# Performance work log

Hardware: AMD Instinct MI355X
Metric: run time of the kernel (lower is better)

## Reference

```python
import jax, jax.numpy as jnp
import numpy as np

# ---- production-scale dims (see shape_source) ----
B, S = 256, 512            # batch, seq_len
HD, INTD = 512, 256        # hidden_dim, hidden_dim // dim_div
N_TEST, N_ITEM, N_TAG = 1500, 9454, 912
N_USER = 7442
GE_ROWS = N_USER + N_ITEM  # LightGCN table: users + items
N_CONT = 3


def _layer_norm(x, g, b, eps=1e-5):
    mu = jnp.mean(x, axis=-1, keepdims=True)
    var = jnp.var(x, axis=-1, keepdims=True)
    return (x - mu) * jax.lax.rsqrt(var + eps) * g + b


def setup_inputs() -> dict:
    key = jax.random.key(0)
    ks = jax.random.split(key, 14)
    f = lambda k, shp, s=0.02: jax.random.normal(k, shp, dtype=jnp.float32) * s
    return {
        # forward data args
        "cate_testId": jax.random.randint(ks[0], (B, S), 0, N_TEST),
        "cate_itemId": jax.random.randint(ks[1], (B, S), 0, N_ITEM),
        "cate_tag": jax.random.randint(ks[2], (B, S), 0, N_TAG),
        "cont_feats": jax.random.normal(ks[3], (B, S, N_CONT), dtype=jnp.float32),
        "interaction": jax.random.randint(ks[4], (B, S), 0, 3),
        # learned parameters
        "emb_interaction": f(ks[5], (3, INTD)),
        "emb_testId": f(ks[6], (N_TEST + 1, INTD)),
        "emb_itemId": f(ks[7], (N_ITEM + 1, INTD)),
        "emb_tag": f(ks[8], (N_TAG + 1, INTD)),
        "graph_table": f(ks[9], (GE_ROWS, HD)),           # pre-trained LightGCN embedding (np.load in torch)
        "graph_W": f(ks[10], (HD, INTD), 0.05),            # graph_linear (in, out) layout
        "graph_b": jnp.zeros((INTD,), jnp.float32),
        "comb_W": f(ks[11], (INTD * 5, HD // 2)),          # intd*(3 cate + 1 graph + interaction)
        "comb_b": jnp.zeros((HD // 2,), jnp.float32),
        "comb_g": jnp.ones((HD // 2,), jnp.float32),
        "comb_beta": jnp.zeros((HD // 2,), jnp.float32),
        "cont_W": f(ks[12], (N_CONT, HD // 2), 0.1),
        "cont_b": jnp.zeros((HD // 2,), jnp.float32),
        "cont_g": jnp.ones((HD // 2,), jnp.float32),
        "cont_beta": jnp.zeros((HD // 2,), jnp.float32),
    }


def reference(cate_testId, cate_itemId, cate_tag, cont_feats, interaction,
              emb_interaction, emb_testId, emb_itemId, emb_tag,
              graph_table, graph_W, graph_b,
              comb_W, comb_b, comb_g, comb_beta,
              cont_W, cont_b, cont_g, cont_beta):
    # categorical + interaction embedding lookups: [B,S,INTD] each
    e_int = emb_interaction[interaction]
    e_test = emb_testId[cate_testId]
    e_item = emb_itemId[cate_itemId]
    e_tag = emb_tag[cate_tag]
    # graph embedding path: fused gather (replaces the CPU python-loop gather)
    # indexes row (n_userID - 1 + value) of the LightGCN table, value from data[0]=testId
    g = graph_table[N_USER - 1 + cate_testId]          # [B,S,HD]
    g = g @ graph_W + graph_b                          # [B,S,INTD]
    embed = jnp.concatenate([e_int, e_test, e_item, e_tag, g], axis=-1)  # [B,S,5*INTD]
    cate = _layer_norm(embed @ comb_W + comb_b, comb_g, comb_beta)       # [B,S,HD//2]
    cont = _layer_norm(cont_feats @ cont_W + cont_b, cont_g, cont_beta)  # [B,S,HD//2]
    return jnp.concatenate([cate, cont], axis=-1)                        # [B,S,HD]
```

## Files before the change

kernel.cpp:

```cpp
#include <hip/hip_runtime.h>
#include <hip/hip_bf16.h>

#define NTOK   (256 * 512)
#define N_USER 7442

using bf16 = __hip_bfloat16;
typedef float f32x4 __attribute__((ext_vector_type(4)));

static __device__ __forceinline__ float4 ld4(const float* p) {
    return *reinterpret_cast<const float4*>(p);
}
static __device__ __forceinline__ float bfl(unsigned u) {
    union { unsigned u; float f; } c; c.u = u << 16; return c.f;
}
static __device__ __forceinline__ float bfh(unsigned u) {
    union { unsigned u; float f; } c; c.u = u & 0xFFFF0000u; return c.f;
}
static __device__ __forceinline__ void st_nt4(float* p, float x, float y, float z, float w) {
    f32x4 v; v.x = x; v.y = y; v.z = z; v.w = w;
    __builtin_nontemporal_store(v, reinterpret_cast<f32x4*>(p));
}
static __device__ __forceinline__ float rnd_bf(float x) {
    return __bfloat162float(__float2bfloat16(x));
}
static __device__ __forceinline__ void st_bf4(bf16* dst, float4 v) {
    union { bf16 h[4]; uint2 u; } pk;
    pk.h[0] = __float2bfloat16(v.x);
    pk.h[1] = __float2bfloat16(v.y);
    pk.h[2] = __float2bfloat16(v.z);
    pk.h[3] = __float2bfloat16(v.w);
    *reinterpret_cast<uint2*>(dst) = pk.u;
}

template <int CTRL, int ROW_MASK>
static __device__ __forceinline__ float dpp_add(float x) {
    const int sh = __builtin_amdgcn_update_dpp(0, __float_as_int(x), CTRL, ROW_MASK, 0xf, true);
    return x + __int_as_float(sh);
}
static __device__ __forceinline__ float wave_sum(float x) {
    x = dpp_add<0x111, 0xf>(x);
    x = dpp_add<0x112, 0xf>(x);
    x = dpp_add<0x114, 0xf>(x);
    x = dpp_add<0x118, 0xf>(x);
    x = dpp_add<0x142, 0xa>(x);
    x = dpp_add<0x143, 0xc>(x);
    return __int_as_float(__builtin_amdgcn_readlane(__float_as_int(x), 63));
}
static __device__ __forceinline__ float dot4(float4 a, float4 b) {
    return a.x * b.x + a.y * b.y + a.z * b.z + a.w * b.w;
}

#define NB_TESTG 188
#define NB_ITEM  591
#define NB_TAG   58
#define NB_INT   1
#define NB_PC    (NB_TESTG + NB_ITEM + NB_TAG + NB_INT)
#define NB_CONT  4096
#define NB_A     (NB_PC + NB_CONT)

__global__ __launch_bounds__(128) void precompute_cont_kernel(
    const float* __restrict__ emb_int,  const float* __restrict__ emb_test,
    const float* __restrict__ emb_item, const float* __restrict__ emb_tag,
    const float* __restrict__ graph_tab, const float* __restrict__ graph_W,
    const float* __restrict__ graph_b,
    const float* __restrict__ comb_W,   const float* __restrict__ comb_b,
    const float* __restrict__ cont_feats,
    const float* __restrict__ cont_W,   const float* __restrict__ cont_b,
    const float* __restrict__ cont_g,   const float* __restrict__ cont_beta,
    bf16* __restrict__ Pint, bf16* __restrict__ Ptestg,
    bf16* __restrict__ Pitem, bf16* __restrict__ Ptag,
    float* __restrict__ Rint, float* __restrict__ Rtestg,
    float* __restrict__ Ritem, float* __restrict__ Rtag,
    float* __restrict__ out) {
    __shared__ float lds[6400];
    const int tid  = threadIdx.x;
    const int w    = tid >> 6;
    const int lane = tid & 63;
    const int c    = lane * 4;
    const int b    = blockIdx.x;

    if (b >= NB_PC) {
        const float4 w0  = ld4(cont_W + 0 * 256 + c);
        const float4 w1  = ld4(cont_W + 1 * 256 + c);
        const float4 w2  = ld4(cont_W + 2 * 256 + c);
        const float4 cb  = ld4(cont_b + c);
        const float4 g42 = ld4(cont_g + c);
        const float4 b42 = ld4(cont_beta + c);

        const float inv256 = 1.f / 256.f;
        const float M0  = wave_sum(w0.x + w0.y + w0.z + w0.w) * inv256;
        const float M1  = wave_sum(w1.x + w1.y + w1.z + w1.w) * inv256;
        const float M2  = wave_sum(w2.x + w2.y + w2.z + w2.w) * inv256;
        const float M3  = wave_sum(cb.x + cb.y + cb.z + cb.w) * inv256;
        const float P00 = wave_sum(dot4(w0, w0)) * inv256;
        const float P11 = wave_sum(dot4(w1, w1)) * inv256;
        const float P22 = wave_sum(dot4(w2, w2)) * inv256;
        const float P33 = wave_sum(dot4(cb, cb)) * inv256;
        const float P01 = wave_sum(dot4(w0, w1)) * inv256;
        const float P02 = wave_sum(dot4(w0, w2)) * inv256;
        const float P12 = wave_sum(dot4(w1, w2)) * inv256;
        const float P03 = wave_sum(dot4(w0, cb)) * inv256;
        const float P13 = wave_sum(dot4(w1, cb)) * inv256;
        const float P23 = wave_sum(dot4(w2, cb)) * inv256;

        const int wid = (b - NB_PC) * 2 + w;
        const int t0  = wid * 16;
        for (int k4 = 0; k4 < 4; ++k4) {
            const int tb = t0 + k4 * 4;
            const float4 cf0 = ld4(cont_feats + (size_t)tb * 3);
            const float4 cf1 = ld4(cont_feats + (size_t)tb * 3 + 4);
            const float4 cf2 = ld4(cont_feats + (size_t)tb * 3 + 8);
            const float cf[12] = {cf0.x, cf0.y, cf0.z, cf0.w,
                                  cf1.x, cf1.y, cf1.z, cf1.w,
                                  cf2.x, cf2.y, cf2.z, cf2.w};
            #pragma unroll
            for (int j = 0; j < 4; ++j) {
                const int t = tb + j;
                const float c0 = cf[j * 3 + 0];
                const float c1 = cf[j * 3 + 1];
                const float c2 = cf[j * 3 + 2];
                const float mu2 = c0 * M0 + c1 * M1 + c2 * M2 + M3;
                const float e2  = c0 * c0 * P00 + c1 * c1 * P11 + c2 * c2 * P22 + P33
                                + 2.f * (c0 * c1 * P01 + c0 * c2 * P02 + c1 * c2 * P12
                                       + c0 * P03 + c1 * P13 + c2 * P23);
                const float inv2 = rsqrtf(e2 - mu2 * mu2 + 1e-5f);

                const float ux = c0 * w0.x + c1 * w1.x + c2 * w2.x + cb.x;
                const float uy = c0 * w0.y + c1 * w1.y + c2 * w2.y + cb.y;
                const float uz = c0 * w0.z + c1 * w1.z + c2 * w2.z + cb.z;
                const float uw = c0 * w0.w + c1 * w1.w + c2 * w2.w + cb.w;

                st_nt4(out + (size_t)t * 512 + 256 + c,
                       (ux - mu2) * inv2 * g42.x + b42.x,
                       (uy - mu2) * inv2 * g42.y + b42.y,
                       (uz - mu2) * inv2 * g42.z + b42.z,
                       (uw - mu2) * inv2 * g42.w + b42.w);
            }
        }
        return;
    }

    const float* W0 = comb_W;
    const float* W1 = comb_W + 256 * 256;
    const float* W2 = comb_W + 512 * 256;
    const float* W3 = comb_W + 768 * 256;
    const float* W4 = comb_W + 1024 * 256;

    if (b < NB_TESTG) {
        const int row0 = b * 8;
        const int nr   = min(8, 1500 - row0);

        for (int i = tid; i < 1024; i += 128) {
            const int r = i >> 7, m4 = (i & 127) * 4;
            const int rr = min(r, nr - 1);
            *reinterpret_cast<float4*>(&lds[r * 512 + m4]) =
                ld4(graph_tab + (size_t)(N_USER - 1 + row0 + rr) * 512 + m4);
        }
        __syncthreads();

        float4 acc[8];
        #pragma unroll
        for (int r = 0; r < 8; ++r) acc[r] = float4{0.f, 0.f, 0.f, 0.f};
        for (int m = w * 256; m < w * 256 + 256; m += 4) {
            const float4 wv0 = ld4(graph_W + (m + 0) * 256 + c);
            const float4 wv1 = ld4(graph_W + (m + 1) * 256 + c);
            const float4 wv2 = ld4(graph_W + (m + 2) * 256 + c);
            const float4 wv3 = ld4(graph_W + (m + 3) * 256 + c);
            #pragma unroll
            for (int r = 0; r < 8; ++r) {
                const float4 e = ld4(&lds[r * 512 + m]);
                acc[r].x += e.x * wv0.x + e.y * wv1.x + e.z * wv2.x + e.w * wv3.x;
                acc[r].y += e.x * wv0.y + e.y * wv1.y + e.z * wv2.y + e.w * wv3.y;
                acc[r].z += e.x * wv0.z + e.y * wv1.z + e.z * wv2.z + e.w * wv3.z;
                acc[r].w += e.x * wv0.w + e.y * wv1.w + e.z * wv2.w + e.w * wv3.w;
            }
        }
        __syncthreads();

        if (w == 0) {
            #pragma unroll
            for (int r = 0; r < 8; ++r)
                *reinterpret_cast<float4*>(&lds[4096 + r * 256 + c]) = acc[r];
        }
        __syncthreads();
        if (w == 1) {
            #pragma unroll
            for (int r = 0; r < 8; ++r) {
                float4 t = ld4(&lds[4096 + r * 256 + c]);
                t.x += acc[r].x; t.y += acc[r].y; t.z += acc[r].z; t.w += acc[r].w;
                *reinterpret_cast<float4*>(&lds[4096 + r * 256 + c]) = t;
            }
        }
        for (int i = tid; i < 512; i += 128) {
            const int r = i >> 6, m4 = (i & 63) * 4;
            const int rr = min(r, nr - 1);
            *reinterpret_cast<float4*>(&lds[r * 256 + m4]) =
                ld4(emb_test + (size_t)(row0 + rr) * 256 + m4);
        }
        __syncthreads();

        float4 acc2[8];
        float4 bacc = float4{0.f, 0.f, 0.f, 0.f};
        #pragma unroll
        for (int r = 0; r < 8; ++r) acc2[r] = float4{0.f, 0.f, 0.f, 0.f};
        for (int m = w * 128; m < w * 128 + 128; m += 4) {
            const float4 w40 = ld4(W4 + (m + 0) * 256 + c);
            const float4 w41 = ld4(W4 + (m + 1) * 256 + c);
            const float4 w42 = ld4(W4 + (m + 2) * 256 + c);
            const float4 w43 = ld4(W4 + (m + 3) * 256 + c);
            const float4 w10 = ld4(W1 + (m + 0) * 256 + c);
            const float4 w11 = ld4(W1 + (m + 1) * 256 + c);
            const float4 w12 = ld4(W1 + (m + 2) * 256 + c);
            const float4 w13 = ld4(W1 + (m + 3) * 256 + c);
            const float gb0 = graph_b[m + 0], gb1 = graph_b[m + 1];
            const float gb2 = graph_b[m + 2], gb3 = graph_b[m + 3];
            bacc.x += gb0 * w40.x + gb1 * w41.x + gb2 * w42.x + gb3 * w43.x;
            bacc.y += gb0 * w40.y + gb1 * w41.y + gb2 * w42.y + gb3 * w43.y;
            bacc.z += gb0 * w40.z + gb1 * w41.z + gb2 * w42.z + gb3 * w43.z;
            bacc.w += gb0 * w40.w + gb1 * w41.w + gb2 * w42.w + gb3 * w43.w;
            #pragma unroll
            for (int r = 0; r < 8; ++r) {
                const float4 tv = ld4(&lds[4096 + r * 256 + m]);
                const float4 ev = ld4(&lds[r * 256 + m]);
                acc2[r].x += tv.x * w40.x + tv.y * w41.x + tv.z * w42.x + tv.w * w43.x
                           + ev.x * w10.x + ev.y * w11.x + ev.z * w12.x + ev.w * w13.x;
                acc2[r].y += tv.x * w40.y + tv.y * w41.y + tv.z * w42.y + tv.w * w43.y
                           + ev.x * w10.y + ev.y * w11.y + ev.z * w12.y + ev.w * w13.y;
                acc2[r].z += tv.x * w40.z + tv.y * w41.z + tv.z * w42.z + tv.w * w43.z
                           + ev.x * w10.z + ev.y * w11.z + ev.z * w12.z + ev.w * w13.z;
                acc2[r].w += tv.x * w40.w + tv.y * w41.w + tv.z * w42.w + tv.w * w43.w
                           + ev.x * w10.w + ev.y * w11.w + ev.z * w12.w + ev.w * w13.w;
            }
        }
        if (w == 0) {
            #pragma unroll
            for (int r = 0; r < 8; ++r)
                *reinterpret_cast<float4*>(&lds[2048 + r * 256 + c]) = acc2[r];
            *reinterpret_cast<float4*>(&lds[6144 + c]) = bacc;
        }
        __syncthreads();
        if (w == 1) {
            #pragma unroll
            for (int r = 0; r < 8; ++r) {
                float4 t = ld4(&lds[2048 + r * 256 + c]);
                t.x += acc2[r].x; t.y += acc2[r].y; t.z += acc2[r].z; t.w += acc2[r].w;
                *reinterpret_cast<float4*>(&lds[2048 + r * 256 + c]) = t;
            }
            float4 t = ld4(&lds[6144 + c]);
            t.x += bacc.x; t.y += bacc.y; t.z += bacc.z; t.w += bacc.w;
            *reinterpret_cast<float4*>(&lds[6144 + c]) = t;
        }
        __syncthreads();

        const float4 cbv = ld4(comb_b + c);
        const float4 bb  = ld4(&lds[6144 + c]);
        #pragma unroll
        for (int r4 = 0; r4 < 4; ++r4) {
            const int r = w * 4 + r4;
            float4 o = ld4(&lds[2048 + r * 256 + c]);
            o.x += bb.x + cbv.x;
            o.y += bb.y + cbv.y;
            o.z += bb.z + cbv.z;
            o.w += bb.w + cbv.w;
            const float rs = wave_sum(rnd_bf(o.x) + rnd_bf(o.y) + rnd_bf(o.z) + rnd_bf(o.w));
            if (r < nr) {
                st_bf4(Ptestg + (size_t)(row0 + r) * 256 + c, o);
                if (lane == 0) Rtestg[row0 + r] = rs;
            }
        }
    } else {
        const float* E; const float* W; bf16* P; float* R; int row0, Rn;
        const int sb = b - NB_TESTG;
        if (sb < NB_ITEM)               { E = emb_item; W = W2; P = Pitem; R = Ritem; row0 = sb * 16;             Rn = 9455; }
        else if (sb < NB_ITEM + NB_TAG) { E = emb_tag;  W = W3; P = Ptag;  R = Rtag;  row0 = (sb - NB_ITEM) * 16; Rn = 913;  }
        else                            { E = emb_int;  W = W0; P = Pint;  R = Rint;  row0 = 0;                   Rn = 3;    }
        const int nr = min(16, Rn - row0);

        for (int i = tid; i < 1024; i += 128) {
            const int r = i >> 6, m4 = (i & 63) * 4;
            const int rr = min(r, nr - 1);
            *reinterpret_cast<float4*>(&lds[r * 256 + m4]) =
                ld4(E + (size_t)(row0 + rr) * 256 + m4);
        }
        __syncthreads();

        float4 acc[16];
        #pragma unroll
        for (int r = 0; r < 16; ++r) acc[r] = float4{0.f, 0.f, 0.f, 0.f};
        for (int m = w * 128; m < w * 128 + 128; m += 4) {
            const float4 wv0 = ld4(W + (m + 0) * 256 + c);
            const float4 wv1 = ld4(W + (m + 1) * 256 + c);
            const float4 wv2 = ld4(W + (m + 2) * 256 + c);
            const float4 wv3 = ld4(W + (m + 3) * 256 + c);
            #pragma unroll
            for (int r = 0; r < 16; ++r) {
                const float4 e = ld4(&lds[r * 256 + m]);
                acc[r].x += e.x * wv0.x + e.y * wv1.x + e.z * wv2.x + e.w * wv3.x;
                acc[r].y += e.x * wv0.y + e.y * wv1.y + e.z * wv2.y + e.w * wv3.y;
                acc[r].z += e.x * wv0.z + e.y * wv1.z + e.z * wv2.z + e.w * wv3.z;
                acc[r].w += e.x * wv0.w + e.y * wv1.w + e.z * wv2.w + e.w * wv3.w;
            }
        }
        __syncthreads();

        if (w == 0) {
            #pragma unroll
            for (int r = 0; r < 16; ++r)
                *reinterpret_cast<float4*>(&lds[r * 256 + c]) = acc[r];
        }
        __syncthreads();
        if (w == 1) {
            #pragma unroll
            for (int r = 0; r < 16; ++r) {
                float4 t = ld4(&lds[r * 256 + c]);
                t.x += acc[r].x; t.y += acc[r].y; t.z += acc[r].z; t.w += acc[r].w;
                *reinterpret_cast<float4*>(&lds[r * 256 + c]) = t;
            }
        }
        __syncthreads();

        #pragma unroll
        for (int r8 = 0; r8 < 8; ++r8) {
            const int r = w * 8 + r8;
            const float4 o = ld4(&lds[r * 256 + c]);
            const float rs = wave_sum(rnd_bf(o.x) + rnd_bf(o.y) + rnd_bf(o.z) + rnd_bf(o.w));
            if (r < nr) {
                st_bf4(P + (size_t)(row0 + r) * 256 + c, o);
                if (lane == 0) R[row0 + r] = rs;
            }
        }
    }
}

__global__ __launch_bounds__(256) void main_cate_kernel(
    const int* __restrict__ testId, const int* __restrict__ itemId,
    const int* __restrict__ tagId,  const int* __restrict__ inter,
    const bf16* __restrict__ Pint, const bf16* __restrict__ Ptestg,
    const bf16* __restrict__ Pitem, const bf16* __restrict__ Ptag,
    const float* __restrict__ Rint, const float* __restrict__ Rtestg,
    const float* __restrict__ Ritem, const float* __restrict__ Rtag,
    const float* __restrict__ comb_g, const float* __restrict__ comb_beta,
    float* __restrict__ out) {
    const int wid  = blockIdx.x * 4 + (threadIdx.x >> 6);
    const int lane = threadIdx.x & 63;
    const int c    = lane * 4;

    const float4 g4 = ld4(comb_g + c);
    const float4 b4 = ld4(comb_beta + c);
    const uint2 p0 = *reinterpret_cast<const uint2*>(Pint + 0 * 256 + c);
    const uint2 p1 = *reinterpret_cast<const uint2*>(Pint + 1 * 256 + c);
    const uint2 p2 = *reinterpret_cast<const uint2*>(Pint + 2 * 256 + c);
    const float ri0 = Rint[0], ri1 = Rint[1], ri2 = Rint[2];

    const int tb = wid * 4;
    const int4 tiv = *reinterpret_cast<const int4*>(testId + tb);
    const int4 iiv = *reinterpret_cast<const int4*>(itemId + tb);
    const int4 tgv = *reinterpret_cast<const int4*>(tagId  + tb);
    const int4 ivv = *reinterpret_cast<const int4*>(inter  + tb);
    const int tis[4] = {tiv.x, tiv.y, tiv.z, tiv.w};
    const int iis[4] = {iiv.x, iiv.y, iiv.z, iiv.w};
    const int tgs[4] = {tgv.x, tgv.y, tgv.z, tgv.w};
    const int ivs[4] = {ivv.x, ivv.y, ivv.z, ivv.w};

    uint2 gT[4], gI[4], gG[4];
    float sT[4], sI[4], sG[4];
    #pragma unroll
    for (int j = 0; j < 4; ++j) {
        gT[j] = *reinterpret_cast<const uint2*>(Ptestg + (size_t)tis[j] * 256 + c);
        gI[j] = *reinterpret_cast<const uint2*>(Pitem  + (size_t)iis[j] * 256 + c);
        gG[j] = *reinterpret_cast<const uint2*>(Ptag   + (size_t)tgs[j] * 256 + c);
        sT[j] = Rtestg[tis[j]];
        sI[j] = Ritem[iis[j]];
        sG[j] = Rtag[tgs[j]];
    }

    #pragma unroll
    for (int j = 0; j < 4; ++j) {
        const int t = tb + j;

        uint2 u0;
        u0.x = ivs[j] == 0 ? p0.x : (ivs[j] == 1 ? p1.x : p2.x);
        u0.y = ivs[j] == 0 ? p0.y : (ivs[j] == 1 ? p1.y : p2.y);
        const float sInt = ivs[j] == 0 ? ri0 : (ivs[j] == 1 ? ri1 : ri2);

        const float vx = bfl(u0.x) + bfl(gT[j].x) + bfl(gI[j].x) + bfl(gG[j].x);
        const float vy = bfh(u0.x) + bfh(gT[j].x) + bfh(gI[j].x) + bfh(gG[j].x);
        const float vz = bfl(u0.y) + bfl(gT[j].y) + bfl(gI[j].y) + bfl(gG[j].y);
        const float vw = bfh(u0.y) + bfh(gT[j].y) + bfh(gI[j].y) + bfh(gG[j].y);

        const float s   = sInt + sT[j] + sI[j] + sG[j];
        const float ss  = wave_sum(vx * vx + vy * vy + vz * vz + vw * vw);
        const float mu  = s * (1.f / 256.f);
        const float var = ss * (1.f / 256.f) - mu * mu;
        const float inv = rsqrtf(var + 1e-5f);

        st_nt4(out + (size_t)t * 512 + c,
               (vx - mu) * inv * g4.x + b4.x,
               (vy - mu) * inv * g4.y + b4.y,
               (vz - mu) * inv * g4.z + b4.z,
               (vw - mu) * inv * g4.w + b4.w);
    }
}

extern "C" void kernel_launch(void* const* d_in, const int* in_sizes, int n_in,
                              void* d_out, int out_size, void* d_ws, size_t ws_size,
                              hipStream_t stream) {
    const int*   testId     = (const int*)d_in[0];
    const int*   itemId     = (const int*)d_in[1];
    const int*   tagId      = (const int*)d_in[2];
    const float* cont_feats = (const float*)d_in[3];
    const int*   inter      = (const int*)d_in[4];
    const float* emb_int    = (const float*)d_in[5];
    const float* emb_test   = (const float*)d_in[6];
    const float* emb_item   = (const float*)d_in[7];
    const float* emb_tag    = (const float*)d_in[8];
    const float* graph_tab  = (const float*)d_in[9];
    const float* graph_W    = (const float*)d_in[10];
    const float* graph_b    = (const float*)d_in[11];
    const float* comb_W     = (const float*)d_in[12];
    const float* comb_b     = (const float*)d_in[13];
    const float* comb_g     = (const float*)d_in[14];
    const float* comb_beta  = (const float*)d_in[15];
    const float* cont_W     = (const float*)d_in[16];
    const float* cont_b     = (const float*)d_in[17];
    const float* cont_g     = (const float*)d_in[18];
    const float* cont_beta  = (const float*)d_in[19];
    float* out              = (float*)d_out;

    bf16* ws     = (bf16*)d_ws;
    bf16* Pitem  = ws;
    bf16* Ptestg = Pitem  + 9455 * 256;
    bf16* Ptag   = Ptestg + 1500 * 256;
    bf16* Pint   = Ptag   +  913 * 256;
    float* Ritem  = (float*)(Pint + 3 * 256);
    float* Rtestg = Ritem  + 9455;
    float* Rtag   = Rtestg + 1500;
    float* Rint   = Rtag   +  913;

    precompute_cont_kernel<<<NB_A, 128, 0, stream>>>(
        emb_int, emb_test, emb_item, emb_tag, graph_tab, graph_W, graph_b,
        comb_W, comb_b, cont_feats, cont_W, cont_b, cont_g, cont_beta,
        Pint, Ptestg, Pitem, Ptag,
        Rint, Rtestg, Ritem, Rtag, out);

    main_cate_kernel<<<NTOK / (4 * 4), 256, 0, stream>>>(
        testId, itemId, tagId, inter,
        Pint, Ptestg, Pitem, Ptag,
        Rint, Rtestg, Ritem, Rtag,
        comb_g, comb_beta, out);
}
```

Measured before the change: 104.1 us.

## Process 16 tokens per wave with software-pipelined gather prefetch

```diff
diff --git a/kernel.cpp b/kernel.cpp
--- a/kernel.cpp
+++ b/kernel.cpp
@@ -352,53 +352,91 @@
     const uint2 p2 = *reinterpret_cast<const uint2*>(Pint + 2 * 256 + c);
     const float ri0 = Rint[0], ri1 = Rint[1], ri2 = Rint[2];
 
-    const int tb = wid * 4;
-    const int4 tiv = *reinterpret_cast<const int4*>(testId + tb);
-    const int4 iiv = *reinterpret_cast<const int4*>(itemId + tb);
-    const int4 tgv = *reinterpret_cast<const int4*>(tagId  + tb);
-    const int4 ivv = *reinterpret_cast<const int4*>(inter  + tb);
-    const int tis[4] = {tiv.x, tiv.y, tiv.z, tiv.w};
-    const int iis[4] = {iiv.x, iiv.y, iiv.z, iiv.w};
-    const int tgs[4] = {tgv.x, tgv.y, tgv.z, tgv.w};
-    const int ivs[4] = {ivv.x, ivv.y, ivv.z, ivv.w};
-
+    const int t0 = wid * 16;
+
+    int   ivs[4];
     uint2 gT[4], gI[4], gG[4];
-    float sT[4], sI[4], sG[4];
+    float sA[4];
+
+    {
+        const int4 tiv = *reinterpret_cast<const int4*>(testId + t0);
+        const int4 iiv = *reinterpret_cast<const int4*>(itemId + t0);
+        const int4 tgv = *reinterpret_cast<const int4*>(tagId  + t0);
+        const int4 ivv = *reinterpret_cast<const int4*>(inter  + t0);
+        const int ti[4] = {tiv.x, tiv.y, tiv.z, tiv.w};
+        const int ii[4] = {iiv.x, iiv.y, iiv.z, iiv.w};
+        const int tg[4] = {tgv.x, tgv.y, tgv.z, tgv.w};
+        ivs[0] = ivv.x; ivs[1] = ivv.y; ivs[2] = ivv.z; ivs[3] = ivv.w;
+        #pragma unroll
+        for (int j = 0; j < 4; ++j) {
+            gT[j] = *reinterpret_cast<const uint2*>(Ptestg + (size_t)ti[j] * 256 + c);
+            gI[j] = *reinterpret_cast<const uint2*>(Pitem  + (size_t)ii[j] * 256 + c);
+            gG[j] = *reinterpret_cast<const uint2*>(Ptag   + (size_t)tg[j] * 256 + c);
+            sA[j] = Rtestg[ti[j]] + Ritem[ii[j]] + Rtag[tg[j]];
+        }
+    }
+
     #pragma unroll
-    for (int j = 0; j < 4; ++j) {
-        gT[j] = *reinterpret_cast<const uint2*>(Ptestg + (size_t)tis[j] * 256 + c);
-        gI[j] = *reinterpret_cast<const uint2*>(Pitem  + (size_t)iis[j] * 256 + c);
-        gG[j] = *reinterpret_cast<const uint2*>(Ptag   + (size_t)tgs[j] * 256 + c);
-        sT[j] = Rtestg[tis[j]];
-        sI[j] = Ritem[iis[j]];
-        sG[j] = Rtag[tgs[j]];
-    }
-
-    #pragma unroll
-    for (int j = 0; j < 4; ++j) {
-        const int t = tb + j;
-
-        uint2 u0;
-        u0.x = ivs[j] == 0 ? p0.x : (ivs[j] == 1 ? p1.x : p2.x);
-        u0.y = ivs[j] == 0 ? p0.y : (ivs[j] == 1 ? p1.y : p2.y);
-        const float sInt = ivs[j] == 0 ? ri0 : (ivs[j] == 1 ? ri1 : ri2);
-
-        const float vx = bfl(u0.x) + bfl(gT[j].x) + bfl(gI[j].x) + bfl(gG[j].x);
-        const float vy = bfh(u0.x) + bfh(gT[j].x) + bfh(gI[j].x) + bfh(gG[j].x);
-        const float vz = bfl(u0.y) + bfl(gT[j].y) + bfl(gI[j].y) + bfl(gG[j].y);
-        const float vw = bfh(u0.y) + bfh(gT[j].y) + bfh(gI[j].y) + bfh(gG[j].y);
-
-        const float s   = sInt + sT[j] + sI[j] + sG[j];
-        const float ss  = wave_sum(vx * vx + vy * vy + vz * vz + vw * vw);
-        const float mu  = s * (1.f / 256.f);
-        const float var = ss * (1.f / 256.f) - mu * mu;
-        const float inv = rsqrtf(var + 1e-5f);
-
-        st_nt4(out + (size_t)t * 512 + c,
-               (vx - mu) * inv * g4.x + b4.x,
-               (vy - mu) * inv * g4.y + b4.y,
-               (vz - mu) * inv * g4.z + b4.z,
-               (vw - mu) * inv * g4.w + b4.w);
+    for (int g = 0; g < 4; ++g) {
+        int   ivsN[4];
+        uint2 gTN[4], gIN[4], gGN[4];
+        float sAN[4];
+        if (g < 3) {
+            const int tb = t0 + (g + 1) * 4;
+            const int4 tiv = *reinterpret_cast<const int4*>(testId + tb);
+            const int4 iiv = *reinterpret_cast<const int4*>(itemId + tb);
+            const int4 tgv = *reinterpret_cast<const int4*>(tagId  + tb);
+            const int4 ivv = *reinterpret_cast<const int4*>(inter  + tb);
+            const int ti[4] = {tiv.x, tiv.y, tiv.z, tiv.w};
+            const int ii[4] = {iiv.x, iiv.y, iiv.z, iiv.w};
+            const int tg[4] = {tgv.x, tgv.y, tgv.z, tgv.w};
+            ivsN[0] = ivv.x; ivsN[1] = ivv.y; ivsN[2] = ivv.z; ivsN[3] = ivv.w;
+            #pragma unroll
+            for (int j = 0; j < 4; ++j) {
+                gTN[j] = *reinterpret_cast<const uint2*>(Ptestg + (size_t)ti[j] * 256 + c);
+                gIN[j] = *reinterpret_cast<const uint2*>(Pitem  + (size_t)ii[j] * 256 + c);
+                gGN[j] = *reinterpret_cast<const uint2*>(Ptag   + (size_t)tg[j] * 256 + c);
+                sAN[j] = Rtestg[ti[j]] + Ritem[ii[j]] + Rtag[tg[j]];
+            }
+        }
+
+        float vx[4], vy[4], vz[4], vw[4], ssv[4], sv[4];
+        #pragma unroll
+        for (int j = 0; j < 4; ++j) {
+            uint2 u0;
+            u0.x = ivs[j] == 0 ? p0.x : (ivs[j] == 1 ? p1.x : p2.x);
+            u0.y = ivs[j] == 0 ? p0.y : (ivs[j] == 1 ? p1.y : p2.y);
+            const float sInt = ivs[j] == 0 ? ri0 : (ivs[j] == 1 ? ri1 : ri2);
+            vx[j] = bfl(u0.x) + bfl(gT[j].x) + bfl(gI[j].x) + bfl(gG[j].x);
+            vy[j] = bfh(u0.x) + bfh(gT[j].x) + bfh(gI[j].x) + bfh(gG[j].x);
+            vz[j] = bfl(u0.y) + bfl(gT[j].y) + bfl(gI[j].y) + bfl(gG[j].y);
+            vw[j] = bfh(u0.y) + bfh(gT[j].y) + bfh(gI[j].y) + bfh(gG[j].y);
+            sv[j]  = sInt + sA[j];
+            ssv[j] = vx[j] * vx[j] + vy[j] * vy[j] + vz[j] * vz[j] + vw[j] * vw[j];
+        }
+        #pragma unroll
+        for (int j = 0; j < 4; ++j) ssv[j] = wave_sum(ssv[j]);
+        #pragma unroll
+        for (int j = 0; j < 4; ++j) {
+            const int t = t0 + g * 4 + j;
+            const float mu  = sv[j] * (1.f / 256.f);
+            const float var = ssv[j] * (1.f / 256.f) - mu * mu;
+            const float inv = rsqrtf(var + 1e-5f);
+            st_nt4(out + (size_t)t * 512 + c,
+                   (vx[j] - mu) * inv * g4.x + b4.x,
+                   (vy[j] - mu) * inv * g4.y + b4.y,
+                   (vz[j] - mu) * inv * g4.z + b4.z,
+                   (vw[j] - mu) * inv * g4.w + b4.w);
+        }
+
+        if (g < 3) {
+            #pragma unroll
+            for (int j = 0; j < 4; ++j) {
+                ivs[j] = ivsN[j];
+                gT[j] = gTN[j]; gI[j] = gIN[j]; gG[j] = gGN[j];
+                sA[j] = sAN[j];
+            }
+        }
     }
 }
 
@@ -443,7 +481,7 @@
         Pint, Ptestg, Pitem, Ptag,
         Rint, Rtestg, Ritem, Rtag, out);
 
-    main_cate_kernel<<<NTOK / (4 * 4), 256, 0, stream>>>(
+    main_cate_kernel<<<NTOK / (4 * 16), 256, 0, stream>>>(
         testId, itemId, tagId, inter,
         Pint, Ptestg, Pitem, Ptag,
         Rint, Rtestg, Ritem, Rtag,
```

Result: no change. 105.5 us (+1.4%).
